# Optimization experiments

Hardware: AMD Instinct MI355X
Metric: run time of the kernel (lower is better)

The kernel has to match this reference:

```python
import jax, jax.numpy as jnp
import numpy as np

IN_CH = 256
IN_SIZE = 64
MID_CH = IN_CH // 2
MID_SIZE = IN_SIZE // 2


def setup_inputs() -> dict:
    key = jax.random.key(0)
    k0, k1, k2, k3, k4 = jax.random.split(key, 5)
    x = jax.random.normal(k0, (32, IN_CH, IN_SIZE, IN_SIZE), dtype=jnp.float32)
    # 1x1 conv weights stored as (out_ch, in_ch); bias=False in the module.
    s_ch = 1.0 / np.sqrt(IN_CH)
    s_sz = 1.0 / np.sqrt(IN_SIZE)
    w_left1 = jax.random.normal(k1, (MID_CH, IN_CH), dtype=jnp.float32) * s_ch
    w_left2 = jax.random.normal(k2, (MID_CH, IN_CH), dtype=jnp.float32) * s_ch
    w_right1 = jax.random.normal(k3, (MID_SIZE, IN_SIZE), dtype=jnp.float32) * s_sz
    w_right2 = jax.random.normal(k4, (MID_SIZE, IN_SIZE), dtype=jnp.float32) * s_sz
    return {"x": x, "w_left1": w_left1, "w_left2": w_left2,
            "w_right1": w_right1, "w_right2": w_right2}


def _att(x, w1, w2):
    # x: (b, c, h, w); w1, w2: (m, c) 1x1-conv weights.
    b, c, h, w = x.shape
    x1 = jnp.einsum('mc,bchw->bmhw', w1, x)          # (b, m, h, w)
    x2 = jnp.mean(x1, axis=(2, 3))                    # adaptive avg pool -> (b, m)
    x3 = jnp.einsum('mc,bchw->bmhw', w2, x).reshape(b, -1, h * w)  # (b, m, hw)
    x4 = jnp.einsum('bm,bmn->bn', x2, x3)             # (b, hw)
    x5 = jax.nn.softmax(x4, axis=-1)
    x6 = jax.nn.sigmoid(x5).reshape(b, 1, h, w)
    return x * x6


def reference(x, w_left1, w_left2, w_right1, w_right2):
    # spatial attention on (b, C, H, W)
    sp = _att(x, w_left1, w_left2)
    # channel attention along H: view (b, H, C, W)
    x1 = jnp.transpose(x, (0, 2, 1, 3))
    ch_h = jnp.transpose(_att(x1, w_right1, w_right2), (0, 2, 1, 3))
    # channel attention along W: view (b, W, H, C)
    x2 = jnp.transpose(x, (0, 3, 2, 1))
    ch_w = jnp.transpose(_att(x2, w_right1, w_right2), (0, 3, 2, 1))
    return sp + ch_h + ch_w
```

## Files before the change

kernel.cpp:

```cpp
#include <hip/hip_runtime.h>
#include <hip/hip_bf16.h>

#define NB 32
#define NC 256
#define NH 64
#define NW 64
#define HW (NH * NW)
#define CHW (NC * NH * NW)

static constexpr size_t OFF_HSUM = 0;
static constexpr size_t OFF_WSUM = OFF_HSUM + (size_t)NB*NC*NH;
static constexpr size_t OFF_CSUM = OFF_WSUM + (size_t)NB*NC*NW;
static constexpr size_t OFF_VSP  = OFF_CSUM + (size_t)NB*NC;
static constexpr size_t OFF_VH   = OFF_VSP  + (size_t)NB*NC;
static constexpr size_t OFF_VW   = OFF_VH   + (size_t)NB*NH;
static constexpr size_t OFF_SSP  = OFF_VW   + (size_t)NB*NW;
static constexpr size_t OFF_SH   = OFF_SSP  + (size_t)NB*HW;
static constexpr size_t OFF_SW   = OFF_SH   + (size_t)NB*NC*NW;
static constexpr size_t OFF_PSP  = OFF_SW   + (size_t)NB*NH*NC;
static constexpr size_t OFF_PSH  = OFF_PSP  + (size_t)NB*HW;
static constexpr size_t OFF_PSW  = OFF_PSH  + (size_t)NB*NC*NW;

__global__ __launch_bounds__(256) void k_stats(const float* __restrict__ x,
                                               float* __restrict__ ws) {
    const int bc = blockIdx.x;
    const int t  = threadIdx.x;
    const float4* plane = reinterpret_cast<const float4*>(x) + ((size_t)bc << 10);
    const float4 v0 = plane[t];
    const float4 v1 = plane[t + 256];
    const float4 v2 = plane[t + 512];
    const float4 v3 = plane[t + 768];
    const int h0 = t >> 4;

    float hp0 = v0.x + v0.y + v0.z + v0.w;
    float hp1 = v1.x + v1.y + v1.z + v1.w;
    float hp2 = v2.x + v2.y + v2.z + v2.w;
    float hp3 = v3.x + v3.y + v3.z + v3.w;
    #pragma unroll
    for (int d = 1; d < 16; d <<= 1) {
        hp0 += __shfl_xor(hp0, d);
        hp1 += __shfl_xor(hp1, d);
        hp2 += __shfl_xor(hp2, d);
        hp3 += __shfl_xor(hp3, d);
    }
    if ((t & 15) == 0) {
        float* hdst = ws + OFF_HSUM + (size_t)bc * NH;
        hdst[h0]      = hp0;
        hdst[h0 + 16] = hp1;
        hdst[h0 + 32] = hp2;
        hdst[h0 + 48] = hp3;
    }

    float4 wp;
    wp.x = v0.x + v1.x + v2.x + v3.x;
    wp.y = v0.y + v1.y + v2.y + v3.y;
    wp.z = v0.z + v1.z + v2.z + v3.z;
    wp.w = v0.w + v1.w + v2.w + v3.w;
    __shared__ float4 red4[256];
    red4[t] = wp;
    __syncthreads();
    for (int s2 = 128; s2 >= 16; s2 >>= 1) {
        if (t < s2) {
            red4[t].x += red4[t + s2].x;
            red4[t].y += red4[t + s2].y;
            red4[t].z += red4[t + s2].z;
            red4[t].w += red4[t + s2].w;
        }
        __syncthreads();
    }
    if (t < 16) {
        reinterpret_cast<float4*>(ws + OFF_WSUM + (size_t)bc * NW)[t] = red4[t];
    }
    if (t == 0) {
        float s = 0.f;
        #pragma unroll
        for (int i = 0; i < 16; ++i)
            s += red4[i].x + red4[i].y + red4[i].z + red4[i].w;
        ws[OFF_CSUM + bc] = s;
    }
}

__global__ __launch_bounds__(256) void k_vecs(const float* __restrict__ wl1,
                                              const float* __restrict__ wl2,
                                              const float* __restrict__ wr1,
                                              const float* __restrict__ wr2,
                                              float* __restrict__ ws) {
    const int b = blockIdx.x, t = threadIdx.x;
    __shared__ float xbc[256], xbh[64], xbw[64], x2sp[128], th[32], tw[32];
    __shared__ float red[256];

    xbc[t] = ws[OFF_CSUM + (size_t)b * NC + t] * (1.0f / 4096.0f);

    {
        const int h = t & 63, part = t >> 6;
        float s = 0.f;
        const float* hs = ws + OFF_HSUM + ((size_t)b * NC + part * 64) * NH + h;
        for (int c = 0; c < 64; ++c) s += hs[(size_t)c * NH];
        red[t] = s;
        __syncthreads();
        if (t < 64) xbh[t] = (red[t] + red[t + 64] + red[t + 128] + red[t + 192]) * (1.0f / 16384.0f);
        __syncthreads();
    }
    {
        const int w = t & 63, part = t >> 6;
        float s = 0.f;
        const float* wsrc = ws + OFF_WSUM + ((size_t)b * NC + part * 64) * NW + w;
        for (int c = 0; c < 64; ++c) s += wsrc[(size_t)c * NW];
        red[t] = s;
        __syncthreads();
        if (t < 64) xbw[t] = (red[t] + red[t + 64] + red[t + 128] + red[t + 192]) * (1.0f / 16384.0f);
        __syncthreads();
    }

    if (t < 128) {
        float a = 0.f;
        for (int c = 0; c < 256; ++c) a += wl1[t * 256 + c] * xbc[c];
        x2sp[t] = a;
    } else if (t < 160) {
        const int m = t - 128;
        float a = 0.f;
        for (int h = 0; h < 64; ++h) a += wr1[m * 64 + h] * xbh[h];
        th[m] = a;
    } else if (t < 192) {
        const int m = t - 160;
        float a = 0.f;
        for (int h = 0; h < 64; ++h) a += wr1[m * 64 + h] * xbw[h];
        tw[m] = a;
    }
    __syncthreads();

    {
        float a = 0.f;
        for (int m = 0; m < 128; ++m) a += x2sp[m] * wl2[m * 256 + t];
        ws[OFF_VSP + (size_t)b * NC + t] = a;
    }
    if (t < 64) {
        float a = 0.f;
        for (int m = 0; m < 32; ++m) a += th[m] * wr2[m * 64 + t];
        ws[OFF_VH + (size_t)b * NH + t] = a;
    } else if (t < 128) {
        const int w = t - 64;
        float a = 0.f;
        for (int m = 0; m < 32; ++m) a += tw[m] * wr2[m * 64 + w];
        ws[OFF_VW + (size_t)b * NW + w] = a;
    }
}

__global__ __launch_bounds__(256) void k_scores(const float* __restrict__ x,
                                                float* __restrict__ ws) {
    const int t = threadIdx.x;
    if (blockIdx.x < 8192) {
        const int bc = blockIdx.x;
        const int b = bc >> 8, c = bc & 255;
        __shared__ float vh_s[64], vw_s[64];
        if (t < 64)        vh_s[t]      = ws[OFF_VH + (size_t)b * NH + t];
        else if (t < 128)  vw_s[t - 64] = ws[OFF_VW + (size_t)b * NW + (t - 64)];
        __syncthreads();

        const float4* plane = reinterpret_cast<const float4*>(x) + ((size_t)bc << 10);
        const float4 v0 = plane[t];
        const float4 v1 = plane[t + 256];
        const float4 v2 = plane[t + 512];
        const float4 v3 = plane[t + 768];
        const int h0 = t >> 4, w4 = t & 15;

        const float4 vwv = reinterpret_cast<const float4*>(vw_s)[w4];
        float hp0 = vwv.x * v0.x + vwv.y * v0.y + vwv.z * v0.z + vwv.w * v0.w;
        float hp1 = vwv.x * v1.x + vwv.y * v1.y + vwv.z * v1.z + vwv.w * v1.w;
        float hp2 = vwv.x * v2.x + vwv.y * v2.y + vwv.z * v2.z + vwv.w * v2.w;
        float hp3 = vwv.x * v3.x + vwv.y * v3.y + vwv.z * v3.z + vwv.w * v3.w;
        #pragma unroll
        for (int d = 1; d < 16; d <<= 1) {
            hp0 += __shfl_xor(hp0, d);
            hp1 += __shfl_xor(hp1, d);
            hp2 += __shfl_xor(hp2, d);
            hp3 += __shfl_xor(hp3, d);
        }
        if ((t & 15) == 0) {
            float* dst = ws + OFF_SW + (size_t)b * NH * NC + c;
            dst[(size_t)(h0)      * NC] = hp0;
            dst[(size_t)(h0 + 16) * NC] = hp1;
            dst[(size_t)(h0 + 32) * NC] = hp2;
            dst[(size_t)(h0 + 48) * NC] = hp3;
        }

        const float a0 = vh_s[h0], a1 = vh_s[h0 + 16], a2 = vh_s[h0 + 32], a3 = vh_s[h0 + 48];
        float4 wp;
        wp.x = a0 * v0.x + a1 * v1.x + a2 * v2.x + a3 * v3.x;
        wp.y = a0 * v0.y + a1 * v1.y + a2 * v2.y + a3 * v3.y;
        wp.z = a0 * v0.z + a1 * v1.z + a2 * v2.z + a3 * v3.z;
        wp.w = a0 * v0.w + a1 * v1.w + a2 * v2.w + a3 * v3.w;
        __shared__ float4 red4[256];
        red4[t] = wp;
        __syncthreads();
        for (int s2 = 128; s2 >= 16; s2 >>= 1) {
            if (t < s2) {
                red4[t].x += red4[t + s2].x;
                red4[t].y += red4[t + s2].y;
                red4[t].z += red4[t + s2].z;
                red4[t].w += red4[t + s2].w;
            }
            __syncthreads();
        }
        if (t < 16) {
            reinterpret_cast<float4*>(ws + OFF_SH + (size_t)bc * NW)[t] = red4[t];
        }
    } else {
        const int idx = blockIdx.x - 8192;
        const int b = idx >> 2, tile = idx & 3;
        __shared__ float vsp[256];
        vsp[t] = ws[OFF_VSP + (size_t)b * NC + t];
        __syncthreads();
        const float4* xb = reinterpret_cast<const float4*>(x) + ((size_t)b << 18);
        const int n4 = tile * 256 + t;
        float4 acc = make_float4(0.f, 0.f, 0.f, 0.f);
        #pragma unroll 4
        for (int c = 0; c < 256; ++c) {
            const float4 xv = xb[(size_t)c * 1024 + n4];
            const float vc = vsp[c];
            acc.x += vc * xv.x;
            acc.y += vc * xv.y;
            acc.z += vc * xv.z;
            acc.w += vc * xv.w;
        }
        reinterpret_cast<float4*>(ws + OFF_SSP + (size_t)b * HW)[n4] = acc;
    }
}

__global__ __launch_bounds__(256) void k_softmax(float* __restrict__ ws) {
    const int blk = blockIdx.x, t = threadIdx.x;
    const int kind = blk >> 5, b = blk & 31;
    const float* src;
    float* dst;
    int N;
    if (kind == 0)      { src = ws + OFF_SSP + (size_t)b * HW;      dst = ws + OFF_PSP + (size_t)b * HW;      N = HW; }
    else if (kind == 1) { src = ws + OFF_SH  + (size_t)b * NC * NW; dst = ws + OFF_PSH + (size_t)b * NC * NW; N = NC * NW; }
    else                { src = ws + OFF_SW  + (size_t)b * NH * NC; dst = ws + OFF_PSW + (size_t)b * NH * NC; N = NH * NC; }

    __shared__ float red[256];
    float mx = -3.4e38f;
    for (int i = t; i < N; i += 256) mx = fmaxf(mx, src[i]);
    red[t] = mx;
    __syncthreads();
    for (int s = 128; s > 0; s >>= 1) {
        if (t < s) red[t] = fmaxf(red[t], red[t + s]);
        __syncthreads();
    }
    mx = red[0];
    __syncthreads();

    float sm = 0.f;
    for (int i = t; i < N; i += 256) sm += expf(src[i] - mx);
    red[t] = sm;
    __syncthreads();
    for (int s = 128; s > 0; s >>= 1) {
        if (t < s) red[t] += red[t + s];
        __syncthreads();
    }
    const float inv = 1.0f / red[0];

    for (int i = t; i < N; i += 256) {
        const float p = expf(src[i] - mx) * inv;
        dst[i] = 1.0f / (1.0f + expf(-p));
    }
}

__global__ __launch_bounds__(256) void k_final(const float* __restrict__ x,
                                               const float* __restrict__ ws,
                                               float* __restrict__ out) {
    const float* psp = ws + OFF_PSP;
    const float* psh = ws + OFF_PSH;
    const float* psw = ws + OFF_PSW;
    const size_t total4 = (size_t)NB * CHW / 4;
    for (size_t i4 = (size_t)blockIdx.x * 256 + threadIdx.x; i4 < total4;
         i4 += (size_t)gridDim.x * 256) {
        const int w4 = (int)(i4 & 15);
        const int h  = (int)((i4 >> 4) & 63);
        const int c  = (int)((i4 >> 10) & 255);
        const int b  = (int)(i4 >> 18);
        const float4 xv = reinterpret_cast<const float4*>(x)[i4];
        const float4 sp = reinterpret_cast<const float4*>(psp)[((size_t)b << 10) + (h << 4) + w4];
        const float4 sh = reinterpret_cast<const float4*>(psh)[(((size_t)b << 8) + c) * 16 + w4];
        const float  sw = psw[((size_t)b << 14) + (h << 8) + c];
        float4 o;
        o.x = xv.x * (sp.x + sh.x + sw);
        o.y = xv.y * (sp.y + sh.y + sw);
        o.z = xv.z * (sp.z + sh.z + sw);
        o.w = xv.w * (sp.w + sh.w + sw);
        reinterpret_cast<float4*>(out)[i4] = o;
    }
}

extern "C" void kernel_launch(void* const* d_in, const int* in_sizes, int n_in,
                              void* d_out, int out_size, void* d_ws, size_t ws_size,
                              hipStream_t stream) {
    const float* x   = (const float*)d_in[0];
    const float* wl1 = (const float*)d_in[1];
    const float* wl2 = (const float*)d_in[2];
    const float* wr1 = (const float*)d_in[3];
    const float* wr2 = (const float*)d_in[4];
    float* out = (float*)d_out;
    float* ws  = (float*)d_ws;

    k_stats  <<<NB * NC, 256, 0, stream>>>(x, ws);
    k_vecs   <<<NB, 256, 0, stream>>>(wl1, wl2, wr1, wr2, ws);
    k_scores <<<NB * NC + NB * 4, 256, 0, stream>>>(x, ws);
    k_softmax<<<3 * NB, 256, 0, stream>>>(ws);
    k_final  <<<2048, 256, 0, stream>>>(x, ws, out);
}
```

Measured before the change: 359.6 us.

## Fuse spatial score computation into per-plane score kernel via partial sums

Removes the separate spatial-score blocks that re-read all of x channel by channel. Each k_scores block now processes 8 channel planes and accumulates the spatial weighted sums in registers, writing per-slice partials that the softmax kernel reduces. This trades a full extra pass over x for a smaller partial-sum buffer and fewer, longer blocks. The final kernel also uses nontemporal output stores and a fixed-count unrolled loop.

Result: faster. 332.1 us (-7.7%).

```diff
diff --git a/kernel.cpp b/kernel.cpp
--- a/kernel.cpp
+++ b/kernel.cpp
@@ -1,12 +1,12 @@
 #include <hip/hip_runtime.h>
-#include <hip/hip_bf16.h>
 
 #define NB 32
 #define NC 256
 #define NH 64
 #define NW 64
 #define HW (NH * NW)
-#define CHW (NC * NH * NW)
+
+typedef float nfloat4 __attribute__((ext_vector_type(4)));
 
 static constexpr size_t OFF_HSUM = 0;
 static constexpr size_t OFF_WSUM = OFF_HSUM + (size_t)NB*NC*NH;
@@ -14,10 +14,10 @@
 static constexpr size_t OFF_VSP  = OFF_CSUM + (size_t)NB*NC;
 static constexpr size_t OFF_VH   = OFF_VSP  + (size_t)NB*NC;
 static constexpr size_t OFF_VW   = OFF_VH   + (size_t)NB*NH;
-static constexpr size_t OFF_SSP  = OFF_VW   + (size_t)NB*NW;
-static constexpr size_t OFF_SH   = OFF_SSP  + (size_t)NB*HW;
+static constexpr size_t OFF_SH   = OFF_VW   + (size_t)NB*NW;
 static constexpr size_t OFF_SW   = OFF_SH   + (size_t)NB*NC*NW;
-static constexpr size_t OFF_PSP  = OFF_SW   + (size_t)NB*NH*NC;
+static constexpr size_t OFF_PART = OFF_SW   + (size_t)NB*NH*NC;
+static constexpr size_t OFF_PSP  = OFF_PART + (size_t)NB*32*HW;
 static constexpr size_t OFF_PSH  = OFF_PSP  + (size_t)NB*HW;
 static constexpr size_t OFF_PSW  = OFF_PSH  + (size_t)NB*NC*NW;
 
@@ -68,9 +68,8 @@
         }
         __syncthreads();
     }
-    if (t < 16) {
+    if (t < 16)
         reinterpret_cast<float4*>(ws + OFF_WSUM + (size_t)bc * NW)[t] = red4[t];
-    }
     if (t == 0) {
         float s = 0.f;
         #pragma unroll
@@ -148,27 +147,38 @@
 
 __global__ __launch_bounds__(256) void k_scores(const float* __restrict__ x,
                                                 float* __restrict__ ws) {
-    const int t = threadIdx.x;
-    if (blockIdx.x < 8192) {
-        const int bc = blockIdx.x;
-        const int b = bc >> 8, c = bc & 255;
-        __shared__ float vh_s[64], vw_s[64];
-        if (t < 64)        vh_s[t]      = ws[OFF_VH + (size_t)b * NH + t];
-        else if (t < 128)  vw_s[t - 64] = ws[OFF_VW + (size_t)b * NW + (t - 64)];
-        __syncthreads();
-
+    const int t   = threadIdx.x;
+    const int blk = blockIdx.x;
+    const int b   = blk >> 5;
+    const int h0  = t >> 4, w4 = t & 15;
+
+    __shared__ float vh_s[64], vw_s[64], vsp_s[256];
+    __shared__ float4 red4[256];
+
+    if (t < 64)       vh_s[t]      = ws[OFF_VH + (size_t)b * NH + t];
+    else if (t < 128) vw_s[t - 64] = ws[OFF_VW + (size_t)b * NW + (t - 64)];
+    vsp_s[t] = ws[OFF_VSP + (size_t)b * NC + t];
+    __syncthreads();
+
+    float4 acc0 = make_float4(0.f,0.f,0.f,0.f);
+    float4 acc1 = make_float4(0.f,0.f,0.f,0.f);
+    float4 acc2 = make_float4(0.f,0.f,0.f,0.f);
+    float4 acc3 = make_float4(0.f,0.f,0.f,0.f);
+
+    for (int p = 0; p < 8; ++p) {
+        const int bc = blk * 8 + p;
+        const int c  = bc & 255;
         const float4* plane = reinterpret_cast<const float4*>(x) + ((size_t)bc << 10);
         const float4 v0 = plane[t];
         const float4 v1 = plane[t + 256];
         const float4 v2 = plane[t + 512];
         const float4 v3 = plane[t + 768];
-        const int h0 = t >> 4, w4 = t & 15;
 
         const float4 vwv = reinterpret_cast<const float4*>(vw_s)[w4];
-        float hp0 = vwv.x * v0.x + vwv.y * v0.y + vwv.z * v0.z + vwv.w * v0.w;
-        float hp1 = vwv.x * v1.x + vwv.y * v1.y + vwv.z * v1.z + vwv.w * v1.w;
-        float hp2 = vwv.x * v2.x + vwv.y * v2.y + vwv.z * v2.z + vwv.w * v2.w;
-        float hp3 = vwv.x * v3.x + vwv.y * v3.y + vwv.z * v3.z + vwv.w * v3.w;
+        float hp0 = vwv.x*v0.x + vwv.y*v0.y + vwv.z*v0.z + vwv.w*v0.w;
+        float hp1 = vwv.x*v1.x + vwv.y*v1.y + vwv.z*v1.z + vwv.w*v1.w;
+        float hp2 = vwv.x*v2.x + vwv.y*v2.y + vwv.z*v2.z + vwv.w*v2.w;
+        float hp3 = vwv.x*v3.x + vwv.y*v3.y + vwv.z*v3.z + vwv.w*v3.w;
         #pragma unroll
         for (int d = 1; d < 16; d <<= 1) {
             hp0 += __shfl_xor(hp0, d);
@@ -176,7 +186,7 @@
             hp2 += __shfl_xor(hp2, d);
             hp3 += __shfl_xor(hp3, d);
         }
-        if ((t & 15) == 0) {
+        if (w4 == 0) {
             float* dst = ws + OFF_SW + (size_t)b * NH * NC + c;
             dst[(size_t)(h0)      * NC] = hp0;
             dst[(size_t)(h0 + 16) * NC] = hp1;
@@ -184,13 +194,12 @@
             dst[(size_t)(h0 + 48) * NC] = hp3;
         }
 
-        const float a0 = vh_s[h0], a1 = vh_s[h0 + 16], a2 = vh_s[h0 + 32], a3 = vh_s[h0 + 48];
+        const float a0 = vh_s[h0], a1 = vh_s[h0+16], a2 = vh_s[h0+32], a3 = vh_s[h0+48];
         float4 wp;
-        wp.x = a0 * v0.x + a1 * v1.x + a2 * v2.x + a3 * v3.x;
-        wp.y = a0 * v0.y + a1 * v1.y + a2 * v2.y + a3 * v3.y;
-        wp.z = a0 * v0.z + a1 * v1.z + a2 * v2.z + a3 * v3.z;
-        wp.w = a0 * v0.w + a1 * v1.w + a2 * v2.w + a3 * v3.w;
-        __shared__ float4 red4[256];
+        wp.x = a0*v0.x + a1*v1.x + a2*v2.x + a3*v3.x;
+        wp.y = a0*v0.y + a1*v1.y + a2*v2.y + a3*v3.y;
+        wp.z = a0*v0.z + a1*v1.z + a2*v2.z + a3*v3.z;
+        wp.w = a0*v0.w + a1*v1.w + a2*v2.w + a3*v3.w;
         red4[t] = wp;
         __syncthreads();
         for (int s2 = 128; s2 >= 16; s2 >>= 1) {
@@ -202,42 +211,94 @@
             }
             __syncthreads();
         }
-        if (t < 16) {
+        if (t < 16)
             reinterpret_cast<float4*>(ws + OFF_SH + (size_t)bc * NW)[t] = red4[t];
-        }
-    } else {
-        const int idx = blockIdx.x - 8192;
-        const int b = idx >> 2, tile = idx & 3;
-        __shared__ float vsp[256];
-        vsp[t] = ws[OFF_VSP + (size_t)b * NC + t];
-        __syncthreads();
-        const float4* xb = reinterpret_cast<const float4*>(x) + ((size_t)b << 18);
-        const int n4 = tile * 256 + t;
-        float4 acc = make_float4(0.f, 0.f, 0.f, 0.f);
-        #pragma unroll 4
-        for (int c = 0; c < 256; ++c) {
-            const float4 xv = xb[(size_t)c * 1024 + n4];
-            const float vc = vsp[c];
-            acc.x += vc * xv.x;
-            acc.y += vc * xv.y;
-            acc.z += vc * xv.z;
-            acc.w += vc * xv.w;
-        }
-        reinterpret_cast<float4*>(ws + OFF_SSP + (size_t)b * HW)[n4] = acc;
-    }
+        __syncthreads();
+
+        const float vc = vsp_s[c];
+        acc0.x += vc*v0.x; acc0.y += vc*v0.y; acc0.z += vc*v0.z; acc0.w += vc*v0.w;
+        acc1.x += vc*v1.x; acc1.y += vc*v1.y; acc1.z += vc*v1.z; acc1.w += vc*v1.w;
+        acc2.x += vc*v2.x; acc2.y += vc*v2.y; acc2.z += vc*v2.z; acc2.w += vc*v2.w;
+        acc3.x += vc*v3.x; acc3.y += vc*v3.y; acc3.z += vc*v3.z; acc3.w += vc*v3.w;
+    }
+
+    float4* pf4 = reinterpret_cast<float4*>(ws + OFF_PART) +
+                  ((size_t)b * 32 + (blk & 31)) * 1024;
+    pf4[t]       = acc0;
+    pf4[t + 256] = acc1;
+    pf4[t + 512] = acc2;
+    pf4[t + 768] = acc3;
 }
 
 __global__ __launch_bounds__(256) void k_softmax(float* __restrict__ ws) {
     const int blk = blockIdx.x, t = threadIdx.x;
     const int kind = blk >> 5, b = blk & 31;
+    __shared__ float red[256];
+    __shared__ float4 ssp4[1024];
+
+    if (kind == 0) {
+        const float4* part = reinterpret_cast<const float4*>(ws + OFF_PART) +
+                             (size_t)b * 32 * 1024;
+        #pragma unroll
+        for (int j = 0; j < 4; ++j) {
+            const int n4 = j * 256 + t;
+            float4 a = make_float4(0.f,0.f,0.f,0.f);
+            for (int s = 0; s < 32; ++s) {
+                const float4 v = part[(size_t)s * 1024 + n4];
+                a.x += v.x; a.y += v.y; a.z += v.z; a.w += v.w;
+            }
+            ssp4[n4] = a;
+        }
+        __syncthreads();
+
+        float mx = -3.4e38f;
+        #pragma unroll
+        for (int j = 0; j < 4; ++j) {
+            const float4 v = ssp4[j * 256 + t];
+            mx = fmaxf(mx, fmaxf(fmaxf(v.x, v.y), fmaxf(v.z, v.w)));
+        }
+        red[t] = mx;
+        __syncthreads();
+        for (int s = 128; s > 0; s >>= 1) {
+            if (t < s) red[t] = fmaxf(red[t], red[t + s]);
+            __syncthreads();
+        }
+        mx = red[0];
+        __syncthreads();
+
+        float sm = 0.f;
+        #pragma unroll
+        for (int j = 0; j < 4; ++j) {
+            const float4 v = ssp4[j * 256 + t];
+            sm += expf(v.x - mx) + expf(v.y - mx) + expf(v.z - mx) + expf(v.w - mx);
+        }
+        red[t] = sm;
+        __syncthreads();
+        for (int s = 128; s > 0; s >>= 1) {
+            if (t < s) red[t] += red[t + s];
+            __syncthreads();
+        }
+        const float inv = 1.0f / red[0];
+        float4* dst = reinterpret_cast<float4*>(ws + OFF_PSP + (size_t)b * HW);
+        #pragma unroll
+        for (int j = 0; j < 4; ++j) {
+            const float4 v = ssp4[j * 256 + t];
+            float4 o;
+            o.x = 1.0f / (1.0f + expf(-(expf(v.x - mx) * inv)));
+            o.y = 1.0f / (1.0f + expf(-(expf(v.y - mx) * inv)));
+            o.z = 1.0f / (1.0f + expf(-(expf(v.z - mx) * inv)));
+            o.w = 1.0f / (1.0f + expf(-(expf(v.w - mx) * inv)));
+            dst[j * 256 + t] = o;
+        }
+        return;
+    }
+
     const float* src;
     float* dst;
-    int N;
-    if (kind == 0)      { src = ws + OFF_SSP + (size_t)b * HW;      dst = ws + OFF_PSP + (size_t)b * HW;      N = HW; }
-    else if (kind == 1) { src = ws + OFF_SH  + (size_t)b * NC * NW; dst = ws + OFF_PSH + (size_t)b * NC * NW; N = NC * NW; }
-    else                { src = ws + OFF_SW  + (size_t)b * NH * NC; dst = ws + OFF_PSW + (size_t)b * NH * NC; N = NH * NC; }
-
-    __shared__ float red[256];
+    const int N = NC * NW;
+    if (kind == 1) { src = ws + OFF_SH + (size_t)b * NC * NW; dst = ws + OFF_PSH + (size_t)b * NC * NW; }
+    else           { src = ws + OFF_SW + (size_t)b * NH * NC; dst = ws + OFF_PSW + (size_t)b * NH * NC; }
+
     float mx = -3.4e38f;
     for (int i = t; i < N; i += 256) mx = fmaxf(mx, src[i]);
     red[t] = mx;
@@ -258,10 +319,9 @@
         __syncthreads();
     }
     const float inv = 1.0f / red[0];
-
     for (int i = t; i < N; i += 256) {
-        const float p = expf(src[i] - mx) * inv;
-        dst[i] = 1.0f / (1.0f + expf(-p));
+        const float pr = expf(src[i] - mx) * inv;
+        dst[i] = 1.0f / (1.0f + expf(-pr));
     }
 }
 
@@ -271,9 +331,10 @@
     const float* psp = ws + OFF_PSP;
     const float* psh = ws + OFF_PSH;
     const float* psw = ws + OFF_PSW;
-    const size_t total4 = (size_t)NB * CHW / 4;
-    for (size_t i4 = (size_t)blockIdx.x * 256 + threadIdx.x; i4 < total4;
-         i4 += (size_t)gridDim.x * 256) {
+    nfloat4* out4 = reinterpret_cast<nfloat4*>(out);
+    size_t i4 = (size_t)blockIdx.x * 256 + threadIdx.x;
+    #pragma unroll 4
+    for (int it = 0; it < 16; ++it, i4 += (size_t)2048 * 256) {
         const int w4 = (int)(i4 & 15);
         const int h  = (int)((i4 >> 4) & 63);
         const int c  = (int)((i4 >> 10) & 255);
@@ -282,12 +343,12 @@
         const float4 sp = reinterpret_cast<const float4*>(psp)[((size_t)b << 10) + (h << 4) + w4];
         const float4 sh = reinterpret_cast<const float4*>(psh)[(((size_t)b << 8) + c) * 16 + w4];
         const float  sw = psw[((size_t)b << 14) + (h << 8) + c];
-        float4 o;
+        nfloat4 o;
         o.x = xv.x * (sp.x + sh.x + sw);
         o.y = xv.y * (sp.y + sh.y + sw);
         o.z = xv.z * (sp.z + sh.z + sw);
         o.w = xv.w * (sp.w + sh.w + sw);
-        reinterpret_cast<float4*>(out)[i4] = o;
+        __builtin_nontemporal_store(o, &out4[i4]);
     }
 }
 
@@ -304,7 +365,7 @@
 
     k_stats  <<<NB * NC, 256, 0, stream>>>(x, ws);
     k_vecs   <<<NB, 256, 0, stream>>>(wl1, wl2, wr1, wr2, ws);
-    k_scores <<<NB * NC + NB * 4, 256, 0, stream>>>(x, ws);
+    k_scores <<<1024, 256, 0, stream>>>(x, ws);
     k_softmax<<<3 * NB, 256, 0, stream>>>(ws);
     k_final  <<<2048, 256, 0, stream>>>(x, ws, out);
 }
```
